# Optimization experiments

Hardware: AMD Instinct MI355X
Metric: run time of the kernel (lower is better)

Reference implementation:

```python
import jax, jax.numpy as jnp
import numpy as np

N, L, S, E, D = 8, 2048, 2048, 1024, 64

def setup_inputs() -> dict:
    key = jax.random.key(0)
    ks = jax.random.split(key, 6)
    q = jax.random.normal(ks[0], (N, L, E), dtype=jnp.float32)
    k = jax.random.normal(ks[1], (N, S, E), dtype=jnp.float32)
    v = jax.random.normal(ks[2], (N, S, E), dtype=jnp.float32)
    # Linear weights stored as [E, D] so projection is x @ W
    Wq = jax.random.normal(ks[3], (E, D), dtype=jnp.float32) / np.sqrt(E)
    Wk = jax.random.normal(ks[4], (E, D), dtype=jnp.float32) / np.sqrt(E)
    Wv = jax.random.normal(ks[5], (E, D), dtype=jnp.float32) / np.sqrt(E)
    # causal bool mask: True above diagonal => masked to -inf
    attn_mask = jnp.triu(jnp.ones((L, S), dtype=bool), k=1)
    return {"q": q, "k": k, "v": v, "Wq": Wq, "Wk": Wk, "Wv": Wv, "attn_mask": attn_mask}


def reference(q, k, v, Wq, Wk, Wv, attn_mask):
    qh = q @ Wq                      # [N, L, D]
    kh = k @ Wk                      # [N, S, D]
    vh = v @ Wv                      # [N, S, D]
    # NOTE: source divides by d**(-1/2), i.e. multiplies by sqrt(D) (faithful bug)
    scale = jnp.asarray(D, dtype=qh.dtype) ** 0.5
    scores = jnp.einsum("nld,nsd->nls", qh, kh) * scale   # [N, L, S]
    scores = jnp.where(attn_mask[None, :, :], -jnp.inf, scores)
    weights = jax.nn.softmax(scores, axis=-1)
    out = jnp.einsum("nls,nsd->nld", weights, vh)          # [N, L, D]
    return out
```

## Files before the change

kernel.cpp:

```cpp
#include <hip/hip_runtime.h>
#include <math.h>

#define NB 8
#define LQ 2048
#define EE 1024
#define DD 64
#define MROWS (NB * LQ)

typedef __attribute__((ext_vector_type(4))) float f32x4;
typedef __attribute__((ext_vector_type(8))) short s16x8;
typedef __attribute__((ext_vector_type(4))) short s16x4;
typedef __attribute__((ext_vector_type(4))) int i32x4;

__device__ __forceinline__ unsigned f2bf_u(float f) {
  unsigned u = __builtin_bit_cast(unsigned, f);
  u += 0x7FFFu + ((u >> 16) & 1u);
  return u >> 16;
}
__device__ __forceinline__ float bf2f(unsigned h) {
  unsigned u = h << 16;
  return __builtin_bit_cast(float, u);
}

__global__ __launch_bounds__(256) void wsplit_kernel(
    const float* __restrict__ Wq, const float* __restrict__ Wk,
    const float* __restrict__ Wv, short* __restrict__ wt) {
  int bk = blockIdx.x;
  int z = blockIdx.y;
  const float* W = (z == 0) ? Wq : (z == 1) ? Wk : Wv;
  __shared__ float tile[64][65];
  int t = threadIdx.x;
#pragma unroll
  for (int it = 0; it < 16; ++it) {
    int kk = it * 4 + (t >> 6);
    int d = t & 63;
    tile[kk][d] = W[(size_t)(bk * 64 + kk) * 64 + d];
  }
  __syncthreads();
#pragma unroll
  for (int it = 0; it < 16; ++it) {
    int d = it * 4 + (t >> 6);
    int kk = t & 63;
    float f = tile[kk][d];
    unsigned h = f2bf_u(f);
    unsigned l = f2bf_u(f - bf2f(h));
    wt[((size_t)(z * 2 + 0) * 64 + d) * 1024 + bk * 64 + kk] = (short)h;
    wt[((size_t)(z * 2 + 1) * 64 + d) * 1024 + bk * 64 + kk] = (short)l;
  }
}

__global__ __launch_bounds__(256, 2) void proj_kernel(
    const float* __restrict__ xq, const float* __restrict__ xk,
    const float* __restrict__ xv, const short* __restrict__ wt,
    int* __restrict__ qkp, short* __restrict__ vhp) {
  int z = blockIdx.y;
  const float* x = (z == 0) ? xq : (z == 1) ? xk : xv;
  const short* wthi = wt + (size_t)(z * 2 + 0) * 64 * 1024;
  const short* wtlo = wt + (size_t)(z * 2 + 1) * 64 * 1024;
  int row0 = blockIdx.x * 128;
  __shared__ short xs_hi[128][72];
  __shared__ short xs_lo[128][72];
  __shared__ short wh[64][72];
  __shared__ short wl[64][72];
  int t = threadIdx.x;
  int wv = t >> 6, lane = t & 63;
  int c = lane & 15, quad = lane >> 4;
  f32x4 acc[2][4] = {};
  for (int kb = 0; kb < 16; ++kb) {
#pragma unroll
    for (int it = 0; it < 8; ++it) {
      int flat4 = it * 256 + t;
      int r = flat4 >> 4, c4 = (flat4 & 15) * 4;
      f32x4 xv4 = *(const f32x4*)&x[(size_t)(row0 + r) * 1024 + kb * 64 + c4];
      s16x4 h, l;
#pragma unroll
      for (int j = 0; j < 4; ++j) {
        unsigned hh = f2bf_u(xv4[j]);
        h[j] = (short)hh;
        l[j] = (short)f2bf_u(xv4[j] - bf2f(hh));
      }
      *(s16x4*)&xs_hi[r][c4] = h;
      *(s16x4*)&xs_lo[r][c4] = l;
    }
#pragma unroll
    for (int it = 0; it < 4; ++it) {
      int flat4 = it * 256 + t;
      int d = flat4 >> 4, k4 = (flat4 & 15) * 4;
      *(s16x4*)&wh[d][k4] = *(const s16x4*)&wthi[(size_t)d * 1024 + kb * 64 + k4];
      *(s16x4*)&wl[d][k4] = *(const s16x4*)&wtlo[(size_t)d * 1024 + kb * 64 + k4];
    }
    __syncthreads();
#pragma unroll
    for (int kc = 0; kc < 2; ++kc) {
      s16x8 ah[2], al[2], bh[4], bl[4];
#pragma unroll
      for (int rs = 0; rs < 2; ++rs) {
        ah[rs] = *(const s16x8*)&xs_hi[wv * 32 + rs * 16 + c][kc * 32 + quad * 8];
        al[rs] = *(const s16x8*)&xs_lo[wv * 32 + rs * 16 + c][kc * 32 + quad * 8];
      }
#pragma unroll
      for (int cs = 0; cs < 4; ++cs) {
        bh[cs] = *(const s16x8*)&wh[cs * 16 + c][kc * 32 + quad * 8];
        bl[cs] = *(const s16x8*)&wl[cs * 16 + c][kc * 32 + quad * 8];
      }
#pragma unroll
      for (int rs = 0; rs < 2; ++rs)
#pragma unroll
        for (int cs = 0; cs < 4; ++cs) {
          acc[rs][cs] = __builtin_amdgcn_mfma_f32_16x16x32_bf16(ah[rs], bh[cs], acc[rs][cs], 0, 0, 0);
          acc[rs][cs] = __builtin_amdgcn_mfma_f32_16x16x32_bf16(ah[rs], bl[cs], acc[rs][cs], 0, 0, 0);
          acc[rs][cs] = __builtin_amdgcn_mfma_f32_16x16x32_bf16(al[rs], bh[cs], acc[rs][cs], 0, 0, 0);
        }
    }
    __syncthreads();
  }
#pragma unroll
  for (int rs = 0; rs < 2; ++rs)
#pragma unroll
    for (int cs = 0; cs < 4; ++cs)
#pragma unroll
      for (int r = 0; r < 4; ++r) {
        int row = row0 + wv * 32 + rs * 16 + quad * 4 + r;
        int col = cs * 16 + c;
        float val = acc[rs][cs][r];
        if (z < 2) {
          unsigned h = f2bf_u(val);
          unsigned l = f2bf_u(val - bf2f(h));
          qkp[(size_t)z * MROWS * 64 + (size_t)row * 64 + col] = (int)(h | (l << 16));
        } else {
          vhp[(size_t)row * 64 + col] = (short)f2bf_u(val);
        }
      }
}

__global__ __launch_bounds__(256) void attn_kernel(
    const int* __restrict__ qkp, const short* __restrict__ vhp,
    float* __restrict__ outp) {
  int qt = blockIdx.x;
  int n = blockIdx.y;
  const int* qp = qkp;
  const int* kp = qkp + (size_t)MROWS * 64;
  __shared__ short ksh[64][72];
  __shared__ short ksl[64][72];
  __shared__ short vT[64][68];
  __shared__ short pS[4][16][72];
  int t = threadIdx.x;
  int wv = t >> 6, lane = t & 63;
  int c = lane & 15, quad = lane >> 4;
  int qr0 = qt * 64;
  s16x8 qfh[2], qfl[2];
  size_t qbase = ((size_t)n * LQ + qr0 + wv * 16 + c) * 64;
#pragma unroll
  for (int kc = 0; kc < 2; ++kc) {
    i32x4 v0 = *(const i32x4*)&qp[qbase + kc * 32 + quad * 8];
    i32x4 v1 = *(const i32x4*)&qp[qbase + kc * 32 + quad * 8 + 4];
#pragma unroll
    for (int j = 0; j < 4; ++j) {
      qfh[kc][j] = (short)(v0[j] & 0xffff);
      qfl[kc][j] = (short)(((unsigned)v0[j]) >> 16);
      qfh[kc][4 + j] = (short)(v1[j] & 0xffff);
      qfl[kc][4 + j] = (short)(((unsigned)v1[j]) >> 16);
    }
  }
  f32x4 o[4] = {};
  float m_r[4], l_r[4];
#pragma unroll
  for (int r = 0; r < 4; ++r) { m_r[r] = -INFINITY; l_r[r] = 0.0f; }

  for (int kt = 0; kt <= qt; ++kt) {
    int s0 = kt * 64;
#pragma unroll
    for (int it = 0; it < 4; ++it) {
      int idx = it * 256 + t;
      int s = idx >> 4, d4 = (idx & 15) * 4;
      size_t g = ((size_t)n * LQ + s0 + s) * 64 + d4;
      i32x4 kv = *(const i32x4*)&kp[g];
      s16x4 h, l;
#pragma unroll
      for (int j = 0; j < 4; ++j) {
        h[j] = (short)(kv[j] & 0xffff);
        l[j] = (short)(((unsigned)kv[j]) >> 16);
      }
      *(s16x4*)&ksh[s][d4] = h;
      *(s16x4*)&ksl[s][d4] = l;
      s16x4 vv = *(const s16x4*)&vhp[g];
#pragma unroll
      for (int j = 0; j < 4; ++j) vT[d4 + j][s] = vv[j];
    }
    __syncthreads();
    f32x4 sa[4] = {};
#pragma unroll
    for (int ct = 0; ct < 4; ++ct) {
#pragma unroll
      for (int kc = 0; kc < 2; ++kc) {
        s16x8 bh = *(const s16x8*)&ksh[ct * 16 + c][kc * 32 + quad * 8];
        s16x8 bl = *(const s16x8*)&ksl[ct * 16 + c][kc * 32 + quad * 8];
        sa[ct] = __builtin_amdgcn_mfma_f32_16x16x32_bf16(qfh[kc], bh, sa[ct], 0, 0, 0);
        sa[ct] = __builtin_amdgcn_mfma_f32_16x16x32_bf16(qfh[kc], bl, sa[ct], 0, 0, 0);
        sa[ct] = __builtin_amdgcn_mfma_f32_16x16x32_bf16(qfl[kc], bh, sa[ct], 0, 0, 0);
      }
    }
    float sv[4][4];
    bool diag = (kt == qt);
#pragma unroll
    for (int ct = 0; ct < 4; ++ct)
#pragma unroll
      for (int r = 0; r < 4; ++r) {
        float xsc = sa[ct][r] * 8.0f;
        if (diag) {
          int sg = s0 + ct * 16 + c;
          int qg = qr0 + wv * 16 + quad * 4 + r;
          if (sg > qg) xsc = -INFINITY;
        }
        sv[ct][r] = xsc;
      }
    float alpha[4];
#pragma unroll
    for (int r = 0; r < 4; ++r) {
      float mx = fmaxf(fmaxf(sv[0][r], sv[1][r]), fmaxf(sv[2][r], sv[3][r]));
#pragma unroll
      for (int off = 1; off < 16; off <<= 1) mx = fmaxf(mx, __shfl_xor(mx, off, 64));
      float mnew = fmaxf(m_r[r], mx);
      alpha[r] = exp2f((m_r[r] - mnew) * 1.44269504088896f);
      m_r[r] = mnew;
      float rs = 0.0f;
#pragma unroll
      for (int ct = 0; ct < 4; ++ct) {
        float p = exp2f((sv[ct][r] - mnew) * 1.44269504088896f);
        sv[ct][r] = p;
        rs += p;
      }
#pragma unroll
      for (int off = 1; off < 16; off <<= 1) rs += __shfl_xor(rs, off, 64);
      l_r[r] = l_r[r] * alpha[r] + rs;
    }
#pragma unroll
    for (int dt = 0; dt < 4; ++dt)
#pragma unroll
      for (int r = 0; r < 4; ++r) o[dt][r] *= alpha[r];
#pragma unroll
    for (int ct = 0; ct < 4; ++ct)
#pragma unroll
      for (int r = 0; r < 4; ++r)
        pS[wv][quad * 4 + r][ct * 16 + c] = (short)f2bf_u(sv[ct][r]);
    s16x8 pa[2];
#pragma unroll
    for (int kc2 = 0; kc2 < 2; ++kc2)
      pa[kc2] = *(const s16x8*)&pS[wv][c][kc2 * 32 + quad * 8];
#pragma unroll
    for (int dt = 0; dt < 4; ++dt) {
#pragma unroll
      for (int kc2 = 0; kc2 < 2; ++kc2) {
        s16x4 v0 = *(const s16x4*)&vT[dt * 16 + c][kc2 * 32 + quad * 8];
        s16x4 v1 = *(const s16x4*)&vT[dt * 16 + c][kc2 * 32 + quad * 8 + 4];
        s16x8 vb;
#pragma unroll
        for (int j = 0; j < 4; ++j) { vb[j] = v0[j]; vb[4 + j] = v1[j]; }
        o[dt] = __builtin_amdgcn_mfma_f32_16x16x32_bf16(pa[kc2], vb, o[dt], 0, 0, 0);
      }
    }
    __syncthreads();
  }
#pragma unroll
  for (int dt = 0; dt < 4; ++dt)
#pragma unroll
    for (int r = 0; r < 4; ++r) {
      int row = qr0 + wv * 16 + quad * 4 + r;
      outp[((size_t)n * LQ + row) * 64 + dt * 16 + c] = o[dt][r] / l_r[r];
    }
}

extern "C" void kernel_launch(void* const* d_in, const int* in_sizes, int n_in,
                              void* d_out, int out_size, void* d_ws, size_t ws_size,
                              hipStream_t stream) {
  const float* q = (const float*)d_in[0];
  const float* k = (const float*)d_in[1];
  const float* v = (const float*)d_in[2];
  const float* Wq = (const float*)d_in[3];
  const float* Wk = (const float*)d_in[4];
  const float* Wv = (const float*)d_in[5];
  float* out = (float*)d_out;

  char* ws = (char*)d_ws;
  short* wt = (short*)ws;
  int* qkp = (int*)(ws + 786432);
  short* vhp = (short*)(ws + 786432 + 8388608);

  wsplit_kernel<<<dim3(16, 3), 256, 0, stream>>>(Wq, Wk, Wv, wt);
  proj_kernel<<<dim3(128, 3), 256, 0, stream>>>(q, k, v, wt, qkp, vhp);
  attn_kernel<<<dim3(32, 8), 256, 0, stream>>>(qkp, vhp, out);
}
```

Baseline: 302.8 us.

## Retile projection with register prefetch, store V transposed, rebalance causal attention grid

The projection kernel now uses 64-row tiles with more blocks and higher occupancy, and it prefetches the next K-slice into registers while the current one is computed. It also skips the lo-split MFMAs for V, since V only needs bf16. V is written out already transposed per batch, so attention can load it into LDS with vector stores instead of scattered transposed writes. Attention is reorganised into 32-row query tiles with 2 waves per block and a grid ordering that pairs short and long causal rows to balance work. The risk is that smaller attention tiles reload each K/V tile twice as often overall.

Measured after the change: 419.2 us. +38.5%, slower.

```diff
diff --git a/kernel.cpp b/kernel.cpp
--- a/kernel.cpp
+++ b/kernel.cpp
@@ -49,105 +49,127 @@
   }
 }
 
-__global__ __launch_bounds__(256, 2) void proj_kernel(
+__global__ __launch_bounds__(256, 4) void proj_kernel(
     const float* __restrict__ xq, const float* __restrict__ xk,
     const float* __restrict__ xv, const short* __restrict__ wt,
-    int* __restrict__ qkp, short* __restrict__ vhp) {
+    int* __restrict__ qkp, short* __restrict__ vhp_t) {
   int z = blockIdx.y;
   const float* x = (z == 0) ? xq : (z == 1) ? xk : xv;
   const short* wthi = wt + (size_t)(z * 2 + 0) * 64 * 1024;
   const short* wtlo = wt + (size_t)(z * 2 + 1) * 64 * 1024;
-  int row0 = blockIdx.x * 128;
-  __shared__ short xs_hi[128][72];
-  __shared__ short xs_lo[128][72];
+  int row0 = blockIdx.x * 64;
+  __shared__ short xs_hi[64][72];
+  __shared__ short xs_lo[64][72];
   __shared__ short wh[64][72];
   __shared__ short wl[64][72];
   int t = threadIdx.x;
   int wv = t >> 6, lane = t & 63;
   int c = lane & 15, quad = lane >> 4;
-  f32x4 acc[2][4] = {};
-  for (int kb = 0; kb < 16; ++kb) {
-#pragma unroll
-    for (int it = 0; it < 8; ++it) {
+  bool split = (z < 2);
+  f32x4 acc[4] = {};
+  f32x4 xr[4];
+  s16x4 wrh[4], wrl[4];
+
+  auto load_tiles = [&](int kb) {
+#pragma unroll
+    for (int it = 0; it < 4; ++it) {
       int flat4 = it * 256 + t;
       int r = flat4 >> 4, c4 = (flat4 & 15) * 4;
-      f32x4 xv4 = *(const f32x4*)&x[(size_t)(row0 + r) * 1024 + kb * 64 + c4];
-      s16x4 h, l;
-#pragma unroll
-      for (int j = 0; j < 4; ++j) {
-        unsigned hh = f2bf_u(xv4[j]);
-        h[j] = (short)hh;
-        l[j] = (short)f2bf_u(xv4[j] - bf2f(hh));
-      }
-      *(s16x4*)&xs_hi[r][c4] = h;
-      *(s16x4*)&xs_lo[r][c4] = l;
-    }
+      xr[it] = *(const f32x4*)&x[(size_t)(row0 + r) * 1024 + kb * 64 + c4];
+      wrh[it] = *(const s16x4*)&wthi[(size_t)r * 1024 + kb * 64 + c4];
+      if (split)
+        wrl[it] = *(const s16x4*)&wtlo[(size_t)r * 1024 + kb * 64 + c4];
+    }
+  };
+
+  load_tiles(0);
+  for (int kb = 0; kb < 16; ++kb) {
 #pragma unroll
     for (int it = 0; it < 4; ++it) {
       int flat4 = it * 256 + t;
-      int d = flat4 >> 4, k4 = (flat4 & 15) * 4;
-      *(s16x4*)&wh[d][k4] = *(const s16x4*)&wthi[(size_t)d * 1024 + kb * 64 + k4];
-      *(s16x4*)&wl[d][k4] = *(const s16x4*)&wtlo[(size_t)d * 1024 + kb * 64 + k4];
-    }
-    __syncthreads();
+      int r = flat4 >> 4, c4 = (flat4 & 15) * 4;
+      s16x4 h, l;
+#pragma unroll
+      for (int j = 0; j < 4; ++j) {
+        unsigned hh = f2bf_u(xr[it][j]);
+        h[j] = (short)hh;
+        l[j] = (short)f2bf_u(xr[it][j] - bf2f(hh));
+      }
+      *(s16x4*)&xs_hi[r][c4] = h;
+      if (split) *(s16x4*)&xs_lo[r][c4] = l;
+      *(s16x4*)&wh[r][c4] = wrh[it];
+      if (split) *(s16x4*)&wl[r][c4] = wrl[it];
+    }
+    __syncthreads();
+    if (kb < 15) load_tiles(kb + 1);
 #pragma unroll
     for (int kc = 0; kc < 2; ++kc) {
-      s16x8 ah[2], al[2], bh[4], bl[4];
-#pragma unroll
-      for (int rs = 0; rs < 2; ++rs) {
-        ah[rs] = *(const s16x8*)&xs_hi[wv * 32 + rs * 16 + c][kc * 32 + quad * 8];
-        al[rs] = *(const s16x8*)&xs_lo[wv * 32 + rs * 16 + c][kc * 32 + quad * 8];
-      }
+      s16x8 ah = *(const s16x8*)&xs_hi[wv * 16 + c][kc * 32 + quad * 8];
+      s16x8 al = {};
+      if (split) al = *(const s16x8*)&xs_lo[wv * 16 + c][kc * 32 + quad * 8];
 #pragma unroll
       for (int cs = 0; cs < 4; ++cs) {
-        bh[cs] = *(const s16x8*)&wh[cs * 16 + c][kc * 32 + quad * 8];
-        bl[cs] = *(const s16x8*)&wl[cs * 16 + c][kc * 32 + quad * 8];
-      }
-#pragma unroll
-      for (int rs = 0; rs < 2; ++rs)
-#pragma unroll
-        for (int cs = 0; cs < 4; ++cs) {
-          acc[rs][cs] = __builtin_amdgcn_mfma_f32_16x16x32_bf16(ah[rs], bh[cs], acc[rs][cs], 0, 0, 0);
-          acc[rs][cs] = __builtin_amdgcn_mfma_f32_16x16x32_bf16(ah[rs], bl[cs], acc[rs][cs], 0, 0, 0);
-          acc[rs][cs] = __builtin_amdgcn_mfma_f32_16x16x32_bf16(al[rs], bh[cs], acc[rs][cs], 0, 0, 0);
+        s16x8 bh = *(const s16x8*)&wh[cs * 16 + c][kc * 32 + quad * 8];
+        acc[cs] = __builtin_amdgcn_mfma_f32_16x16x32_bf16(ah, bh, acc[cs], 0, 0, 0);
+        if (split) {
+          s16x8 bl = *(const s16x8*)&wl[cs * 16 + c][kc * 32 + quad * 8];
+          acc[cs] = __builtin_amdgcn_mfma_f32_16x16x32_bf16(ah, bl, acc[cs], 0, 0, 0);
+          acc[cs] = __builtin_amdgcn_mfma_f32_16x16x32_bf16(al, bh, acc[cs], 0, 0, 0);
         }
-    }
-    __syncthreads();
-  }
-#pragma unroll
-  for (int rs = 0; rs < 2; ++rs)
+      }
+    }
+    __syncthreads();
+  }
+  if (split) {
 #pragma unroll
     for (int cs = 0; cs < 4; ++cs)
 #pragma unroll
       for (int r = 0; r < 4; ++r) {
-        int row = row0 + wv * 32 + rs * 16 + quad * 4 + r;
+        int row = row0 + wv * 16 + quad * 4 + r;
         int col = cs * 16 + c;
-        float val = acc[rs][cs][r];
-        if (z < 2) {
-          unsigned h = f2bf_u(val);
-          unsigned l = f2bf_u(val - bf2f(h));
-          qkp[(size_t)z * MROWS * 64 + (size_t)row * 64 + col] = (int)(h | (l << 16));
-        } else {
-          vhp[(size_t)row * 64 + col] = (short)f2bf_u(val);
-        }
-      }
-}
-
-__global__ __launch_bounds__(256) void attn_kernel(
-    const int* __restrict__ qkp, const short* __restrict__ vhp,
+        float val = acc[cs][r];
+        unsigned h = f2bf_u(val);
+        unsigned l = f2bf_u(val - bf2f(h));
+        qkp[(size_t)z * MROWS * 64 + (size_t)row * 64 + col] = (int)(h | (l << 16));
+      }
+  } else {
+#pragma unroll
+    for (int cs = 0; cs < 4; ++cs)
+#pragma unroll
+      for (int r = 0; r < 4; ++r)
+        xs_hi[wv * 16 + quad * 4 + r][cs * 16 + c] = (short)f2bf_u(acc[cs][r]);
+    __syncthreads();
+    int n = row0 >> 11;
+    int s0l = row0 & 2047;
+#pragma unroll
+    for (int it = 0; it < 4; ++it) {
+      int flat4 = it * 256 + t;
+      int d = flat4 >> 4, s4 = (flat4 & 15) * 4;
+      s16x4 vv;
+#pragma unroll
+      for (int j = 0; j < 4; ++j) vv[j] = xs_hi[s4 + j][d];
+      *(s16x4*)&vhp_t[((size_t)n * 64 + d) * 2048 + s0l + s4] = vv;
+    }
+  }
+}
+
+__global__ __launch_bounds__(128) void attn_kernel(
+    const int* __restrict__ qkp, const short* __restrict__ vhp_t,
     float* __restrict__ outp) {
-  int qt = blockIdx.x;
-  int n = blockIdx.y;
+  int n = blockIdx.x;
+  int y = blockIdx.y;
+  int qt2 = (y < 32) ? y : (95 - y);
+  int qr0 = qt2 * 32;
+  int nk = qt2 / 2 + 1;
   const int* qp = qkp;
   const int* kp = qkp + (size_t)MROWS * 64;
   __shared__ short ksh[64][72];
   __shared__ short ksl[64][72];
-  __shared__ short vT[64][68];
-  __shared__ short pS[4][16][72];
+  __shared__ short vT[64][72];
+  __shared__ short pS[2][16][72];
   int t = threadIdx.x;
   int wv = t >> 6, lane = t & 63;
   int c = lane & 15, quad = lane >> 4;
-  int qr0 = qt * 64;
   s16x8 qfh[2], qfl[2];
   size_t qbase = ((size_t)n * LQ + qr0 + wv * 16 + c) * 64;
 #pragma unroll
@@ -167,14 +189,13 @@
 #pragma unroll
   for (int r = 0; r < 4; ++r) { m_r[r] = -INFINITY; l_r[r] = 0.0f; }
 
-  for (int kt = 0; kt <= qt; ++kt) {
+  for (int kt = 0; kt < nk; ++kt) {
     int s0 = kt * 64;
 #pragma unroll
-    for (int it = 0; it < 4; ++it) {
-      int idx = it * 256 + t;
-      int s = idx >> 4, d4 = (idx & 15) * 4;
-      size_t g = ((size_t)n * LQ + s0 + s) * 64 + d4;
-      i32x4 kv = *(const i32x4*)&kp[g];
+    for (int it = 0; it < 8; ++it) {
+      int flat4 = it * 128 + t;
+      int s = flat4 >> 4, d4 = (flat4 & 15) * 4;
+      i32x4 kv = *(const i32x4*)&kp[((size_t)n * LQ + s0 + s) * 64 + d4];
       s16x4 h, l;
 #pragma unroll
       for (int j = 0; j < 4; ++j) {
@@ -183,9 +204,13 @@
       }
       *(s16x4*)&ksh[s][d4] = h;
       *(s16x4*)&ksl[s][d4] = l;
-      s16x4 vv = *(const s16x4*)&vhp[g];
-#pragma unroll
-      for (int j = 0; j < 4; ++j) vT[d4 + j][s] = vv[j];
+    }
+#pragma unroll
+    for (int it = 0; it < 8; ++it) {
+      int flat4 = it * 128 + t;
+      int d = flat4 >> 4, s4 = (flat4 & 15) * 4;
+      *(s16x4*)&vT[d][s4] =
+          *(const s16x4*)&vhp_t[((size_t)n * 64 + d) * 2048 + s0 + s4];
     }
     __syncthreads();
     f32x4 sa[4] = {};
@@ -201,7 +226,7 @@
       }
     }
     float sv[4][4];
-    bool diag = (kt == qt);
+    bool diag = (kt == nk - 1);
 #pragma unroll
     for (int ct = 0; ct < 4; ++ct)
 #pragma unroll
@@ -284,9 +309,9 @@
   char* ws = (char*)d_ws;
   short* wt = (short*)ws;
   int* qkp = (int*)(ws + 786432);
-  short* vhp = (short*)(ws + 786432 + 8388608);
+  short* vhp_t = (short*)(ws + 786432 + 8388608);
 
   wsplit_kernel<<<dim3(16, 3), 256, 0, stream>>>(Wq, Wk, Wv, wt);
-  proj_kernel<<<dim3(128, 3), 256, 0, stream>>>(q, k, v, wt, qkp, vhp);
-  attn_kernel<<<dim3(32, 8), 256, 0, stream>>>(qkp, vhp, out);
-}
+  proj_kernel<<<dim3(256, 3), 256, 0, stream>>>(q, k, v, wt, qkp, vhp_t);
+  attn_kernel<<<dim3(8, 64), 128, 0, stream>>>(qkp, vhp_t, out);
+}
```

## Split attention KV across blocks with combine pass and per-wave projection tiles

Applied to the files above, without the earlier changes.

The projection kernel now gives each wave its own 16-row tile. It reads x and the weights straight from global memory into registers, prefetches the next k-chunk, and drops shared memory staging and block barriers. V is computed with only the hi weight term and is written transposed. The attention kernel now works per wave, with each wave handling a 16-row query group. It splits the KV range into up to four chunks, reads K and transposed V directly from global memory without shared staging, and computes the row sum with an MFMA against a ones vector. A new combine kernel merges the partial outputs using their max and sum values. The aim is to balance the causal workload and add parallelism, at the cost of extra partial-output traffic and one more launch.

After: 363.8 us. 1.2x slower.

```diff
diff --git a/kernel.cpp b/kernel.cpp
--- a/kernel.cpp
+++ b/kernel.cpp
@@ -6,6 +6,7 @@
 #define EE 1024
 #define DD 64
 #define MROWS (NB * LQ)
+#define L2E 1.44269504088896f
 
 typedef __attribute__((ext_vector_type(4))) float f32x4;
 typedef __attribute__((ext_vector_type(8))) short s16x8;
@@ -49,107 +50,124 @@
   }
 }
 
-__global__ __launch_bounds__(256, 2) void proj_kernel(
+__global__ __launch_bounds__(256, 3) void proj_kernel(
     const float* __restrict__ xq, const float* __restrict__ xk,
     const float* __restrict__ xv, const short* __restrict__ wt,
-    int* __restrict__ qkp, short* __restrict__ vhp) {
-  int z = blockIdx.y;
-  const float* x = (z == 0) ? xq : (z == 1) ? xk : xv;
-  const short* wthi = wt + (size_t)(z * 2 + 0) * 64 * 1024;
-  const short* wtlo = wt + (size_t)(z * 2 + 1) * 64 * 1024;
-  int row0 = blockIdx.x * 128;
-  __shared__ short xs_hi[128][72];
-  __shared__ short xs_lo[128][72];
-  __shared__ short wh[64][72];
-  __shared__ short wl[64][72];
+    int* __restrict__ qkp, short* __restrict__ vhp_t) {
+  __shared__ short vls[4][16][68];
   int t = threadIdx.x;
   int wv = t >> 6, lane = t & 63;
   int c = lane & 15, quad = lane >> 4;
-  f32x4 acc[2][4] = {};
+  int w = blockIdx.x * 4 + wv;
+  int z = w >> 10;
+  int rowg = w & 1023;
+  const float* x = (z == 0) ? xq : (z == 1) ? xk : xv;
+  const short* wthi = wt + (size_t)(z * 2) * 64 * 1024;
+  const short* wtlo = wthi + 64 * 1024;
+  bool split = (z < 2);
+  const float* xr = x + (size_t)(rowg * 16 + c) * 1024;
+
+  f32x4 acc[4] = {};
+  f32x4 cur[2][2], nxt[2][2];
+#pragma unroll
+  for (int kc = 0; kc < 2; ++kc) {
+    cur[kc][0] = *(const f32x4*)&xr[kc * 32 + quad * 8];
+    cur[kc][1] = *(const f32x4*)&xr[kc * 32 + quad * 8 + 4];
+  }
   for (int kb = 0; kb < 16; ++kb) {
-#pragma unroll
-    for (int it = 0; it < 8; ++it) {
-      int flat4 = it * 256 + t;
-      int r = flat4 >> 4, c4 = (flat4 & 15) * 4;
-      f32x4 xv4 = *(const f32x4*)&x[(size_t)(row0 + r) * 1024 + kb * 64 + c4];
-      s16x4 h, l;
-#pragma unroll
-      for (int j = 0; j < 4; ++j) {
-        unsigned hh = f2bf_u(xv4[j]);
-        h[j] = (short)hh;
-        l[j] = (short)f2bf_u(xv4[j] - bf2f(hh));
-      }
-      *(s16x4*)&xs_hi[r][c4] = h;
-      *(s16x4*)&xs_lo[r][c4] = l;
-    }
-#pragma unroll
-    for (int it = 0; it < 4; ++it) {
-      int flat4 = it * 256 + t;
-      int d = flat4 >> 4, k4 = (flat4 & 15) * 4;
-      *(s16x4*)&wh[d][k4] = *(const s16x4*)&wthi[(size_t)d * 1024 + kb * 64 + k4];
-      *(s16x4*)&wl[d][k4] = *(const s16x4*)&wtlo[(size_t)d * 1024 + kb * 64 + k4];
-    }
-    __syncthreads();
-#pragma unroll
-    for (int kc = 0; kc < 2; ++kc) {
-      s16x8 ah[2], al[2], bh[4], bl[4];
-#pragma unroll
-      for (int rs = 0; rs < 2; ++rs) {
-        ah[rs] = *(const s16x8*)&xs_hi[wv * 32 + rs * 16 + c][kc * 32 + quad * 8];
-        al[rs] = *(const s16x8*)&xs_lo[wv * 32 + rs * 16 + c][kc * 32 + quad * 8];
-      }
-#pragma unroll
-      for (int cs = 0; cs < 4; ++cs) {
-        bh[cs] = *(const s16x8*)&wh[cs * 16 + c][kc * 32 + quad * 8];
-        bl[cs] = *(const s16x8*)&wl[cs * 16 + c][kc * 32 + quad * 8];
-      }
-#pragma unroll
-      for (int rs = 0; rs < 2; ++rs)
-#pragma unroll
-        for (int cs = 0; cs < 4; ++cs) {
-          acc[rs][cs] = __builtin_amdgcn_mfma_f32_16x16x32_bf16(ah[rs], bh[cs], acc[rs][cs], 0, 0, 0);
-          acc[rs][cs] = __builtin_amdgcn_mfma_f32_16x16x32_bf16(ah[rs], bl[cs], acc[rs][cs], 0, 0, 0);
-          acc[rs][cs] = __builtin_amdgcn_mfma_f32_16x16x32_bf16(al[rs], bh[cs], acc[rs][cs], 0, 0, 0);
+    if (kb < 15) {
+#pragma unroll
+      for (int kc = 0; kc < 2; ++kc) {
+        nxt[kc][0] = *(const f32x4*)&xr[(kb + 1) * 64 + kc * 32 + quad * 8];
+        nxt[kc][1] = *(const f32x4*)&xr[(kb + 1) * 64 + kc * 32 + quad * 8 + 4];
+      }
+    }
+    s16x8 ah[2], al[2];
+#pragma unroll
+    for (int kc = 0; kc < 2; ++kc)
+#pragma unroll
+      for (int h = 0; h < 2; ++h)
+#pragma unroll
+        for (int j = 0; j < 4; ++j) {
+          float f = cur[kc][h][j];
+          unsigned hh = f2bf_u(f);
+          ah[kc][h * 4 + j] = (short)hh;
+          al[kc][h * 4 + j] = (short)f2bf_u(f - bf2f(hh));
         }
-    }
-    __syncthreads();
-  }
-#pragma unroll
-  for (int rs = 0; rs < 2; ++rs)
+#pragma unroll
+    for (int cs = 0; cs < 4; ++cs) {
+      const short* bp = wthi + (size_t)(cs * 16 + c) * 1024 + kb * 64 + quad * 8;
+      s16x8 bh0 = *(const s16x8*)bp;
+      s16x8 bh1 = *(const s16x8*)(bp + 32);
+      acc[cs] = __builtin_amdgcn_mfma_f32_16x16x32_bf16(ah[0], bh0, acc[cs], 0, 0, 0);
+      acc[cs] = __builtin_amdgcn_mfma_f32_16x16x32_bf16(ah[1], bh1, acc[cs], 0, 0, 0);
+      if (split) {
+        const short* bpl = wtlo + (size_t)(cs * 16 + c) * 1024 + kb * 64 + quad * 8;
+        s16x8 bl0 = *(const s16x8*)bpl;
+        s16x8 bl1 = *(const s16x8*)(bpl + 32);
+        acc[cs] = __builtin_amdgcn_mfma_f32_16x16x32_bf16(ah[0], bl0, acc[cs], 0, 0, 0);
+        acc[cs] = __builtin_amdgcn_mfma_f32_16x16x32_bf16(al[0], bh0, acc[cs], 0, 0, 0);
+        acc[cs] = __builtin_amdgcn_mfma_f32_16x16x32_bf16(ah[1], bl1, acc[cs], 0, 0, 0);
+        acc[cs] = __builtin_amdgcn_mfma_f32_16x16x32_bf16(al[1], bh1, acc[cs], 0, 0, 0);
+      }
+    }
+#pragma unroll
+    for (int kc = 0; kc < 2; ++kc)
+#pragma unroll
+      for (int h = 0; h < 2; ++h) cur[kc][h] = nxt[kc][h];
+  }
+  if (split) {
 #pragma unroll
     for (int cs = 0; cs < 4; ++cs)
 #pragma unroll
       for (int r = 0; r < 4; ++r) {
-        int row = row0 + wv * 32 + rs * 16 + quad * 4 + r;
-        int col = cs * 16 + c;
-        float val = acc[rs][cs][r];
-        if (z < 2) {
-          unsigned h = f2bf_u(val);
-          unsigned l = f2bf_u(val - bf2f(h));
-          qkp[(size_t)z * MROWS * 64 + (size_t)row * 64 + col] = (int)(h | (l << 16));
-        } else {
-          vhp[(size_t)row * 64 + col] = (short)f2bf_u(val);
-        }
-      }
-}
-
-__global__ __launch_bounds__(256) void attn_kernel(
-    const int* __restrict__ qkp, const short* __restrict__ vhp,
-    float* __restrict__ outp) {
-  int qt = blockIdx.x;
-  int n = blockIdx.y;
-  const int* qp = qkp;
-  const int* kp = qkp + (size_t)MROWS * 64;
-  __shared__ short ksh[64][72];
-  __shared__ short ksl[64][72];
-  __shared__ short vT[64][68];
+        int row = rowg * 16 + quad * 4 + r;
+        float val = acc[cs][r];
+        unsigned h = f2bf_u(val);
+        unsigned l = f2bf_u(val - bf2f(h));
+        qkp[(size_t)z * MROWS * 64 + (size_t)row * 64 + cs * 16 + c] =
+            (int)(h | (l << 16));
+      }
+  } else {
+#pragma unroll
+    for (int cs = 0; cs < 4; ++cs)
+#pragma unroll
+      for (int r = 0; r < 4; ++r)
+        vls[wv][quad * 4 + r][cs * 16 + c] = (short)f2bf_u(acc[cs][r]);
+    int n = rowg >> 7;
+    int sb = (rowg * 16) & 2047;
+    s16x8 p0, p1;
+#pragma unroll
+    for (int j = 0; j < 8; ++j) {
+      p0[j] = vls[wv][j][lane];
+      p1[j] = vls[wv][8 + j][lane];
+    }
+    *(s16x8*)&vhp_t[((size_t)n * 64 + lane) * 2048 + sb] = p0;
+    *(s16x8*)&vhp_t[((size_t)n * 64 + lane) * 2048 + sb + 8] = p1;
+  }
+}
+
+__global__ __launch_bounds__(256, 3) void attn_kernel(
+    const int* __restrict__ qkp, const short* __restrict__ vhp_t,
+    float* __restrict__ po, float* __restrict__ pm, float* __restrict__ pl,
+    int S) {
   __shared__ short pS[4][16][72];
   int t = threadIdx.x;
   int wv = t >> 6, lane = t & 63;
   int c = lane & 15, quad = lane >> 4;
-  int qr0 = qt * 64;
+  int w = blockIdx.x * 4 + wv;
+  int qg = w & 1023;
+  int split = w >> 10;
+  int n = qg >> 7;
+  int qgl = qg & 127;
+  int nk = (qgl >> 2) + 1;
+  int dk = qgl >> 2;
+  int k0 = (split * nk) / S, k1 = ((split + 1) * nk) / S;
+  const int* qp = qkp;
+  const int* kp = qkp + (size_t)MROWS * 64;
+
   s16x8 qfh[2], qfl[2];
-  size_t qbase = ((size_t)n * LQ + qr0 + wv * 16 + c) * 64;
+  size_t qbase = (size_t)(qg * 16 + c) * 64;
 #pragma unroll
   for (int kc = 0; kc < 2; ++kc) {
     i32x4 v0 = *(const i32x4*)&qp[qbase + kc * 32 + quad * 8];
@@ -162,46 +180,47 @@
       qfl[kc][4 + j] = (short)(((unsigned)v1[j]) >> 16);
     }
   }
+  s16x8 ones;
+#pragma unroll
+  for (int j = 0; j < 8; ++j) ones[j] = (short)0x3F80;
   f32x4 o[4] = {};
-  float m_r[4], l_r[4];
-#pragma unroll
-  for (int r = 0; r < 4; ++r) { m_r[r] = -INFINITY; l_r[r] = 0.0f; }
-
-  for (int kt = 0; kt <= qt; ++kt) {
+  f32x4 lsum = {};
+  float m_r[4];
+#pragma unroll
+  for (int r = 0; r < 4; ++r) m_r[r] = -INFINITY;
+
+  for (int kt = k0; kt < k1; ++kt) {
     int s0 = kt * 64;
-#pragma unroll
-    for (int it = 0; it < 4; ++it) {
-      int idx = it * 256 + t;
-      int s = idx >> 4, d4 = (idx & 15) * 4;
-      size_t g = ((size_t)n * LQ + s0 + s) * 64 + d4;
-      i32x4 kv = *(const i32x4*)&kp[g];
-      s16x4 h, l;
-#pragma unroll
-      for (int j = 0; j < 4; ++j) {
-        h[j] = (short)(kv[j] & 0xffff);
-        l[j] = (short)(((unsigned)kv[j]) >> 16);
-      }
-      *(s16x4*)&ksh[s][d4] = h;
-      *(s16x4*)&ksl[s][d4] = l;
-      s16x4 vv = *(const s16x4*)&vhp[g];
-#pragma unroll
-      for (int j = 0; j < 4; ++j) vT[d4 + j][s] = vv[j];
-    }
-    __syncthreads();
+    s16x8 vf[4][2];
+#pragma unroll
+    for (int dt = 0; dt < 4; ++dt)
+#pragma unroll
+      for (int kc2 = 0; kc2 < 2; ++kc2)
+        vf[dt][kc2] = *(const s16x8*)&vhp_t[((size_t)n * 64 + dt * 16 + c) * 2048 +
+                                            s0 + kc2 * 32 + quad * 8];
     f32x4 sa[4] = {};
 #pragma unroll
     for (int ct = 0; ct < 4; ++ct) {
+      const int* krow = &kp[((size_t)n * 2048 + s0 + ct * 16 + c) * 64];
 #pragma unroll
       for (int kc = 0; kc < 2; ++kc) {
-        s16x8 bh = *(const s16x8*)&ksh[ct * 16 + c][kc * 32 + quad * 8];
-        s16x8 bl = *(const s16x8*)&ksl[ct * 16 + c][kc * 32 + quad * 8];
+        i32x4 p0 = *(const i32x4*)&krow[kc * 32 + quad * 8];
+        i32x4 p1 = *(const i32x4*)&krow[kc * 32 + quad * 8 + 4];
+        s16x8 bh, bl;
+#pragma unroll
+        for (int j = 0; j < 4; ++j) {
+          bh[j] = (short)(p0[j] & 0xffff);
+          bl[j] = (short)(((unsigned)p0[j]) >> 16);
+          bh[4 + j] = (short)(p1[j] & 0xffff);
+          bl[4 + j] = (short)(((unsigned)p1[j]) >> 16);
+        }
         sa[ct] = __builtin_amdgcn_mfma_f32_16x16x32_bf16(qfh[kc], bh, sa[ct], 0, 0, 0);
         sa[ct] = __builtin_amdgcn_mfma_f32_16x16x32_bf16(qfh[kc], bl, sa[ct], 0, 0, 0);
         sa[ct] = __builtin_amdgcn_mfma_f32_16x16x32_bf16(qfl[kc], bh, sa[ct], 0, 0, 0);
       }
     }
     float sv[4][4];
-    bool diag = (kt == qt);
+    bool diag = (kt == dk);
 #pragma unroll
     for (int ct = 0; ct < 4; ++ct)
 #pragma unroll
@@ -209,8 +228,8 @@
         float xsc = sa[ct][r] * 8.0f;
         if (diag) {
           int sg = s0 + ct * 16 + c;
-          int qg = qr0 + wv * 16 + quad * 4 + r;
-          if (sg > qg) xsc = -INFINITY;
+          int qgr = qgl * 16 + quad * 4 + r;
+          if (sg > qgr) xsc = -INFINITY;
         }
         sv[ct][r] = xsc;
       }
@@ -221,23 +240,18 @@
 #pragma unroll
       for (int off = 1; off < 16; off <<= 1) mx = fmaxf(mx, __shfl_xor(mx, off, 64));
       float mnew = fmaxf(m_r[r], mx);
-      alpha[r] = exp2f((m_r[r] - mnew) * 1.44269504088896f);
+      alpha[r] = exp2f((m_r[r] - mnew) * L2E);
       m_r[r] = mnew;
-      float rs = 0.0f;
-#pragma unroll
-      for (int ct = 0; ct < 4; ++ct) {
-        float p = exp2f((sv[ct][r] - mnew) * 1.44269504088896f);
-        sv[ct][r] = p;
-        rs += p;
-      }
-#pragma unroll
-      for (int off = 1; off < 16; off <<= 1) rs += __shfl_xor(rs, off, 64);
-      l_r[r] = l_r[r] * alpha[r] + rs;
+#pragma unroll
+      for (int ct = 0; ct < 4; ++ct)
+        sv[ct][r] = exp2f((sv[ct][r] - mnew) * L2E);
     }
 #pragma unroll
     for (int dt = 0; dt < 4; ++dt)
 #pragma unroll
       for (int r = 0; r < 4; ++r) o[dt][r] *= alpha[r];
+#pragma unroll
+    for (int r = 0; r < 4; ++r) lsum[r] *= alpha[r];
 #pragma unroll
     for (int ct = 0; ct < 4; ++ct)
 #pragma unroll
@@ -247,27 +261,50 @@
 #pragma unroll
     for (int kc2 = 0; kc2 < 2; ++kc2)
       pa[kc2] = *(const s16x8*)&pS[wv][c][kc2 * 32 + quad * 8];
+    lsum = __builtin_amdgcn_mfma_f32_16x16x32_bf16(pa[0], ones, lsum, 0, 0, 0);
+    lsum = __builtin_amdgcn_mfma_f32_16x16x32_bf16(pa[1], ones, lsum, 0, 0, 0);
 #pragma unroll
     for (int dt = 0; dt < 4; ++dt) {
-#pragma unroll
-      for (int kc2 = 0; kc2 < 2; ++kc2) {
-        s16x4 v0 = *(const s16x4*)&vT[dt * 16 + c][kc2 * 32 + quad * 8];
-        s16x4 v1 = *(const s16x4*)&vT[dt * 16 + c][kc2 * 32 + quad * 8 + 4];
-        s16x8 vb;
-#pragma unroll
-        for (int j = 0; j < 4; ++j) { vb[j] = v0[j]; vb[4 + j] = v1[j]; }
-        o[dt] = __builtin_amdgcn_mfma_f32_16x16x32_bf16(pa[kc2], vb, o[dt], 0, 0, 0);
-      }
-    }
-    __syncthreads();
-  }
+      o[dt] = __builtin_amdgcn_mfma_f32_16x16x32_bf16(pa[0], vf[dt][0], o[dt], 0, 0, 0);
+      o[dt] = __builtin_amdgcn_mfma_f32_16x16x32_bf16(pa[1], vf[dt][1], o[dt], 0, 0, 0);
+    }
+  }
+  int rb = qg * 16 + quad * 4;
 #pragma unroll
   for (int dt = 0; dt < 4; ++dt)
 #pragma unroll
+    for (int r = 0; r < 4; ++r)
+      po[((size_t)split * MROWS + rb + r) * 64 + dt * 16 + c] = o[dt][r];
+  if (c == 0) {
+#pragma unroll
     for (int r = 0; r < 4; ++r) {
-      int row = qr0 + wv * 16 + quad * 4 + r;
-      outp[((size_t)n * LQ + row) * 64 + dt * 16 + c] = o[dt][r] / l_r[r];
-    }
+      pm[(size_t)split * MROWS + rb + r] = m_r[r];
+      pl[(size_t)split * MROWS + rb + r] = lsum[r];
+    }
+  }
+}
+
+__global__ __launch_bounds__(256) void combine_kernel(
+    const float* __restrict__ po, const float* __restrict__ pm,
+    const float* __restrict__ pl, float* __restrict__ outp, int S) {
+  int id = blockIdx.x * 256 + threadIdx.x;
+  int row = id >> 4;
+  int c4 = (id & 15) * 4;
+  float M = -INFINITY;
+  for (int s = 0; s < S; ++s) M = fmaxf(M, pm[(size_t)s * MROWS + row]);
+  float den = 0.0f;
+  f32x4 acc = {};
+  for (int s = 0; s < S; ++s) {
+    float wgt = exp2f((pm[(size_t)s * MROWS + row] - M) * L2E);
+    den += pl[(size_t)s * MROWS + row] * wgt;
+    f32x4 pv = *(const f32x4*)&po[((size_t)s * MROWS + row) * 64 + c4];
+#pragma unroll
+    for (int j = 0; j < 4; ++j) acc[j] += pv[j] * wgt;
+  }
+  f32x4 res;
+#pragma unroll
+  for (int j = 0; j < 4; ++j) res[j] = acc[j] / den;
+  *(f32x4*)&outp[(size_t)row * 64 + c4] = res;
 }
 
 extern "C" void kernel_launch(void* const* d_in, const int* in_sizes, int n_in,
@@ -282,11 +319,23 @@
   float* out = (float*)d_out;
 
   char* ws = (char*)d_ws;
+  size_t base = 786432 + 8388608 + 2097152;
+  size_t po_sz = (size_t)MROWS * 64 * 4;
+  size_t ml_sz = (size_t)MROWS * 4;
+  size_t per_split = po_sz + 2 * ml_sz;
+  int S = 1;
+  if (ws_size >= base + 4 * per_split) S = 4;
+  else if (ws_size >= base + 2 * per_split) S = 2;
+
   short* wt = (short*)ws;
   int* qkp = (int*)(ws + 786432);
-  short* vhp = (short*)(ws + 786432 + 8388608);
+  short* vhp_t = (short*)(ws + 786432 + 8388608);
+  float* po = (float*)(ws + base);
+  float* pm = (float*)(ws + base + (size_t)S * po_sz);
+  float* pl = (float*)(ws + base + (size_t)S * po_sz + (size_t)S * ml_sz);
 
   wsplit_kernel<<<dim3(16, 3), 256, 0, stream>>>(Wq, Wk, Wv, wt);
-  proj_kernel<<<dim3(128, 3), 256, 0, stream>>>(q, k, v, wt, qkp, vhp);
-  attn_kernel<<<dim3(32, 8), 256, 0, stream>>>(qkp, vhp, out);
-}
+  proj_kernel<<<dim3(768), 256, 0, stream>>>(q, k, v, wt, qkp, vhp_t);
+  attn_kernel<<<dim3(256 * S), 256, 0, stream>>>(qkp, vhp_t, po, pm, pl, S);
+  combine_kernel<<<dim3(1024), 256, 0, stream>>>(po, pm, pl, out, S);
+}
```
